# Optimization experiments

Hardware: AMD Instinct MI355X
Metric: run time of the kernel (lower is better)

The kernel has to match this reference:

```python
import jax, jax.numpy as jnp
import numpy as np

# Each of the 16 soft logic gates g(a,b) is affine in {1, a, b, a*b}.
# COEFF[g] = [k0, ka, kb, kab] so that gate_g = k0 + ka*a + kb*b + kab*a*b.
COEFF = np.array([
    [0,  0,  0,  0],   # 0: False
    [0,  0,  0,  1],   # 1: a AND b
    [0,  1,  0, -1],   # 2: a AND NOT b
    [0,  1,  0,  0],   # 3: a
    [0,  0,  1, -1],   # 4: NOT a AND b
    [0,  0,  1,  0],   # 5: b
    [0,  1,  1, -2],   # 6: XOR
    [0,  1,  1, -1],   # 7: OR
    [1, -1, -1,  1],   # 8: NOR
    [1, -1, -1,  2],   # 9: XNOR
    [1,  0, -1,  0],   # 10: NOT b
    [1,  0, -1,  1],   # 11: a OR NOT b
    [1, -1,  0,  0],   # 12: NOT a
    [1, -1,  0,  1],   # 13: NOT a OR b
    [1,  0,  0, -1],   # 14: NAND
    [1,  0,  0,  0],   # 15: True
], dtype=np.float32)

BATCH, IN_DIM, OUT_DIM, N_GATES = 2048, 16384, 16384, 16


def setup_inputs() -> dict:
    key = jax.random.key(0)
    k1, k2, k3, k4 = jax.random.split(key, 4)
    x = jax.random.uniform(k1, (BATCH, IN_DIM), dtype=jnp.float32)
    weights = jax.random.normal(k2, (OUT_DIM, N_GATES), dtype=jnp.float32)
    idx_a = jax.random.randint(k3, (OUT_DIM,), 0, IN_DIM, dtype=jnp.int64)
    idx_b = jax.random.randint(k4, (OUT_DIM,), 0, IN_DIM, dtype=jnp.int64)
    return {"x": x, "weights": weights, "idx_a": idx_a, "idx_b": idx_b}


def reference(x, weights, idx_a, idx_b):
    # Training-mode forward: softmax mixture over the 16 logic gates.
    nw = jax.nn.softmax(weights, axis=-1)            # [out, 16]
    W = nw @ jnp.asarray(COEFF, dtype=x.dtype)       # [out, 4] effective affine coeffs
    a = x[:, idx_a]                                  # [batch, out]
    b = x[:, idx_b]                                  # [batch, out]
    ab = a * b
    # r = sum_g nw[:,g] * gate_g(a,b) == W0 + Wa*a + Wb*b + Wab*ab
    return W[:, 0] + W[:, 1] * a + W[:, 2] * b + W[:, 3] * ab
```

## Files before the change

kernel.cpp:

```cpp
#include <hip/hip_runtime.h>

#define BATCH   2048
#define IN_DIM  16384
#define OUT_DIM 16384
#define NGATES  16

typedef float    f32x4 __attribute__((ext_vector_type(4)));
typedef _Float16 f16x4 __attribute__((ext_vector_type(4)));
typedef _Float16 f16x8 __attribute__((ext_vector_type(8)));

__constant__ float c_coeff[NGATES][4] = {
    {0, 0, 0, 0},  {0, 0, 0, 1},  {0, 1, 0, -1}, {0, 1, 0, 0},
    {0, 0, 1, -1}, {0, 0, 1, 0},  {0, 1, 1, -2}, {0, 1, 1, -1},
    {1, -1, -1, 1},{1, -1, -1, 2},{1, 0, -1, 0}, {1, 0, -1, 1},
    {1, -1, 0, 0}, {1, -1, 0, 1}, {1, 0, 0, -1}, {1, 0, 0, 0}
};

__global__ __launch_bounds__(256) void prep_kernel(
    const float* __restrict__ weights,
    const int*   __restrict__ idx_a,
    const int*   __restrict__ idx_b,
    f16x4*       __restrict__ Wh,
    unsigned*    __restrict__ Ipk)
{
    int j = blockIdx.x * blockDim.x + threadIdx.x;
    if (j >= OUT_DIM) return;

    const float4* wrow = reinterpret_cast<const float4*>(weights + (size_t)j * NGATES);
    float v[NGATES];
    float4 q0 = wrow[0], q1 = wrow[1], q2 = wrow[2], q3 = wrow[3];
    v[0]=q0.x; v[1]=q0.y; v[2]=q0.z; v[3]=q0.w;
    v[4]=q1.x; v[5]=q1.y; v[6]=q1.z; v[7]=q1.w;
    v[8]=q2.x; v[9]=q2.y; v[10]=q2.z; v[11]=q2.w;
    v[12]=q3.x; v[13]=q3.y; v[14]=q3.z; v[15]=q3.w;

    float m = v[0];
#pragma unroll
    for (int g = 1; g < NGATES; ++g) m = fmaxf(m, v[g]);
    float s = 0.f;
#pragma unroll
    for (int g = 0; g < NGATES; ++g) { v[g] = expf(v[g] - m); s += v[g]; }
    float inv = 1.0f / s;

    float c0 = 0.f, c1 = 0.f, c2 = 0.f, c3 = 0.f;
#pragma unroll
    for (int g = 0; g < NGATES; ++g) {
        c0 += v[g] * c_coeff[g][0];
        c1 += v[g] * c_coeff[g][1];
        c2 += v[g] * c_coeff[g][2];
        c3 += v[g] * c_coeff[g][3];
    }
    f16x4 h;
    h.x = (_Float16)(c0 * inv); h.y = (_Float16)(c1 * inv);
    h.z = (_Float16)(c2 * inv); h.w = (_Float16)(c3 * inv);
    Wh[j] = h;
    Ipk[j] = (unsigned)idx_a[j] | ((unsigned)idx_b[j] << 16);
}

__global__ __launch_bounds__(512, 8) void logic_row_kernel(
    const float* __restrict__ x,
    const f16x8* __restrict__ Wh8,
    const uint4* __restrict__ Ipk4,
    float*       __restrict__ out)
{
    __shared__ _Float16 rowh[IN_DIM];
    const int tid = threadIdx.x;
    const int i   = blockIdx.x;

    const f32x4* xr  = reinterpret_cast<const f32x4*>(x + (size_t)i * IN_DIM);
    f16x4*       rhw = reinterpret_cast<f16x4*>(rowh);
#pragma unroll
    for (int k = 0; k < IN_DIM / 4 / 512; ++k) {
        f32x4 v = xr[tid + k * 512];
        f16x4 h;
        h.x = (_Float16)v.x; h.y = (_Float16)v.y;
        h.z = (_Float16)v.z; h.w = (_Float16)v.w;
        rhw[tid + k * 512] = h;
    }

    uint4 qc = Ipk4[tid];
    f16x8 wa = Wh8[(size_t)tid * 2];
    f16x8 wb = Wh8[(size_t)tid * 2 + 1];

    __syncthreads();

    f32x4* o4 = reinterpret_cast<f32x4*>(out + (size_t)i * OUT_DIM);

    for (int k = 0; k < OUT_DIM / 4 / 512; ++k) {
        uint4 qn;  f16x8 wan, wbn;
        if (k + 1 < OUT_DIM / 4 / 512) {
            const int j4n = tid + (k + 1) * 512;
            qn  = Ipk4[j4n];
            wan = Wh8[(size_t)j4n * 2];
            wbn = Wh8[(size_t)j4n * 2 + 1];
        }

        float a0 = (float)rowh[qc.x & 0xFFFFu], b0 = (float)rowh[qc.x >> 16];
        float a1 = (float)rowh[qc.y & 0xFFFFu], b1 = (float)rowh[qc.y >> 16];
        float a2 = (float)rowh[qc.z & 0xFFFFu], b2 = (float)rowh[qc.z >> 16];
        float a3 = (float)rowh[qc.w & 0xFFFFu], b3 = (float)rowh[qc.w >> 16];

        f32x4 res;
        res.x = (float)wa[0] + (float)wa[1] * a0 + (float)wa[2] * b0 + (float)wa[3] * (a0 * b0);
        res.y = (float)wa[4] + (float)wa[5] * a1 + (float)wa[6] * b1 + (float)wa[7] * (a1 * b1);
        res.z = (float)wb[0] + (float)wb[1] * a2 + (float)wb[2] * b2 + (float)wb[3] * (a2 * b2);
        res.w = (float)wb[4] + (float)wb[5] * a3 + (float)wb[6] * b3 + (float)wb[7] * (a3 * b3);
        __builtin_nontemporal_store(res, &o4[tid + k * 512]);

        qc = qn; wa = wan; wb = wbn;
    }
}

extern "C" void kernel_launch(void* const* d_in, const int* in_sizes, int n_in,
                              void* d_out, int out_size, void* d_ws, size_t ws_size,
                              hipStream_t stream) {
    const float* x       = (const float*)d_in[0];
    const float* weights = (const float*)d_in[1];
    const int*   idx_a   = (const int*)d_in[2];
    const int*   idx_b   = (const int*)d_in[3];
    float* out = (float*)d_out;

    f16x4*    Wh  = (f16x4*)d_ws;
    unsigned* Ipk = (unsigned*)((char*)d_ws + (size_t)OUT_DIM * sizeof(f16x4));

    prep_kernel<<<(OUT_DIM + 255) / 256, 256, 0, stream>>>(weights, idx_a, idx_b, Wh, Ipk);
    logic_row_kernel<<<BATCH, 512, 0, stream>>>(x, (const f16x8*)Wh, (const uint4*)Ipk, out);
}
```

Before: 49.14 us.

## Process two rows per block, prefetching the next x row during compute

Each block now handles two batch rows. The second row of x is loaded into registers while the first row is being computed, and the converted fp16 row is reused from LDS. The grid shrinks to half as many blocks, and the compute loop is now fully unrolled. The aim is to hide the global load latency of the x row behind gather compute. In exchange, register pressure rises (8 f32x4 held across compute_row), which may cut occupancy under launch_bounds(512,8), and the kernel exposes less parallelism.

```diff
diff --git a/kernel.cpp b/kernel.cpp
--- a/kernel.cpp
+++ b/kernel.cpp
@@ -4,6 +4,8 @@
 #define IN_DIM  16384
 #define OUT_DIM 16384
 #define NGATES  16
+#define ROWS_PER_BLOCK 2
+#define NBLK (BATCH / ROWS_PER_BLOCK)
 
 typedef float    f32x4 __attribute__((ext_vector_type(4)));
 typedef _Float16 f16x4 __attribute__((ext_vector_type(4)));
@@ -57,35 +59,18 @@
     Ipk[j] = (unsigned)idx_a[j] | ((unsigned)idx_b[j] << 16);
 }
 
-__global__ __launch_bounds__(512, 8) void logic_row_kernel(
-    const float* __restrict__ x,
+__device__ __forceinline__ void compute_row(
+    const _Float16* __restrict__ rowh,
     const f16x8* __restrict__ Wh8,
     const uint4* __restrict__ Ipk4,
-    float*       __restrict__ out)
+    float* __restrict__ orow, int tid)
 {
-    __shared__ _Float16 rowh[IN_DIM];
-    const int tid = threadIdx.x;
-    const int i   = blockIdx.x;
-
-    const f32x4* xr  = reinterpret_cast<const f32x4*>(x + (size_t)i * IN_DIM);
-    f16x4*       rhw = reinterpret_cast<f16x4*>(rowh);
-#pragma unroll
-    for (int k = 0; k < IN_DIM / 4 / 512; ++k) {
-        f32x4 v = xr[tid + k * 512];
-        f16x4 h;
-        h.x = (_Float16)v.x; h.y = (_Float16)v.y;
-        h.z = (_Float16)v.z; h.w = (_Float16)v.w;
-        rhw[tid + k * 512] = h;
-    }
-
     uint4 qc = Ipk4[tid];
     f16x8 wa = Wh8[(size_t)tid * 2];
     f16x8 wb = Wh8[(size_t)tid * 2 + 1];
+    f32x4* o4 = reinterpret_cast<f32x4*>(orow);
 
-    __syncthreads();
-
-    f32x4* o4 = reinterpret_cast<f32x4*>(out + (size_t)i * OUT_DIM);
-
+#pragma unroll
     for (int k = 0; k < OUT_DIM / 4 / 512; ++k) {
         uint4 qn;  f16x8 wan, wbn;
         if (k + 1 < OUT_DIM / 4 / 512) {
@@ -111,6 +96,55 @@
     }
 }
 
+__global__ __launch_bounds__(512, 8) void logic_row_kernel(
+    const float* __restrict__ x,
+    const f16x8* __restrict__ Wh8,
+    const uint4* __restrict__ Ipk4,
+    float*       __restrict__ out)
+{
+    __shared__ _Float16 rowh[IN_DIM];
+    const int tid = threadIdx.x;
+    const int r0  = blockIdx.x * ROWS_PER_BLOCK;
+
+    f16x4* rhw = reinterpret_cast<f16x4*>(rowh);
+    f32x4  s[8];
+
+    {
+        const f32x4* xr = reinterpret_cast<const f32x4*>(x + (size_t)r0 * IN_DIM);
+#pragma unroll
+        for (int k = 0; k < 8; ++k) s[k] = xr[tid + k * 512];
+#pragma unroll
+        for (int k = 0; k < 8; ++k) {
+            f16x4 h;
+            h.x = (_Float16)s[k].x; h.y = (_Float16)s[k].y;
+            h.z = (_Float16)s[k].z; h.w = (_Float16)s[k].w;
+            rhw[tid + k * 512] = h;
+        }
+    }
+    __syncthreads();
+
+    {
+        const f32x4* xr = reinterpret_cast<const f32x4*>(x + (size_t)(r0 + 1) * IN_DIM);
+#pragma unroll
+        for (int k = 0; k < 8; ++k) s[k] = xr[tid + k * 512];
+    }
+
+    compute_row(rowh, Wh8, Ipk4, out + (size_t)r0 * OUT_DIM, tid);
+
+    __syncthreads();
+
+#pragma unroll
+    for (int k = 0; k < 8; ++k) {
+        f16x4 h;
+        h.x = (_Float16)s[k].x; h.y = (_Float16)s[k].y;
+        h.z = (_Float16)s[k].z; h.w = (_Float16)s[k].w;
+        rhw[tid + k * 512] = h;
+    }
+    __syncthreads();
+
+    compute_row(rowh, Wh8, Ipk4, out + (size_t)(r0 + 1) * OUT_DIM, tid);
+}
+
 extern "C" void kernel_launch(void* const* d_in, const int* in_sizes, int n_in,
                               void* d_out, int out_size, void* d_ws, size_t ws_size,
                               hipStream_t stream) {
@@ -124,5 +158,5 @@
     unsigned* Ipk = (unsigned*)((char*)d_ws + (size_t)OUT_DIM * sizeof(f16x4));
 
     prep_kernel<<<(OUT_DIM + 255) / 256, 256, 0, stream>>>(weights, idx_a, idx_b, Wh, Ipk);
-    logic_row_kernel<<<BATCH, 512, 0, stream>>>(x, (const f16x8*)Wh, (const uint4*)Ipk, out);
+    logic_row_kernel<<<NBLK, 512, 0, stream>>>(x, (const f16x8*)Wh, (const uint4*)Ipk, out);
 }
```

After: 56.74 us. +15.5%, slower.

## Double-buffer x rows in LDS with async global_load_lds across rows

Applied to the files above, without the earlier changes.

Each block now processes 8 batch rows with 1024 threads. It stages the next x row into a second LDS buffer using direct global-to-LDS loads while the current row is gathered and computed. Rows are kept in fp32 in LDS, which drops the fp16 conversion but doubles LDS use to 128KB per block, and the grid shrinks to 256 blocks. The per-block Wh/Ipk loads are amortised over rows, but occupancy and block count drop sharply. Barrier timing around the async loads could also be fragile.

```diff
diff --git a/kernel.cpp b/kernel.cpp
--- a/kernel.cpp
+++ b/kernel.cpp
@@ -4,6 +4,8 @@
 #define IN_DIM  16384
 #define OUT_DIM 16384
 #define NGATES  16
+#define ROWS_PER_BLOCK 8
+#define NBLK (BATCH / ROWS_PER_BLOCK)
 
 typedef float    f32x4 __attribute__((ext_vector_type(4)));
 typedef _Float16 f16x4 __attribute__((ext_vector_type(4)));
@@ -57,57 +59,77 @@
     Ipk[j] = (unsigned)idx_a[j] | ((unsigned)idx_b[j] << 16);
 }
 
-__global__ __launch_bounds__(512, 8) void logic_row_kernel(
-    const float* __restrict__ x,
+__device__ __forceinline__ void stage_row_async(const float* __restrict__ xrow,
+                                                float* lbuf, int tid)
+{
+#pragma unroll
+    for (int kk = 0; kk < 4; ++kk) {
+        __builtin_amdgcn_global_load_lds(
+            (const __attribute__((address_space(1))) void*)(xrow + tid * 4 + kk * 4096),
+            (__attribute__((address_space(3))) void*)(lbuf + tid * 4 + kk * 4096),
+            16, 0, 0);
+    }
+}
+
+__device__ __forceinline__ void compute_row(
+    const float* __restrict__ rowf,
     const f16x8* __restrict__ Wh8,
     const uint4* __restrict__ Ipk4,
-    float*       __restrict__ out)
+    float* __restrict__ orow, int tid)
 {
-    __shared__ _Float16 rowh[IN_DIM];
-    const int tid = threadIdx.x;
-    const int i   = blockIdx.x;
-
-    const f32x4* xr  = reinterpret_cast<const f32x4*>(x + (size_t)i * IN_DIM);
-    f16x4*       rhw = reinterpret_cast<f16x4*>(rowh);
-#pragma unroll
-    for (int k = 0; k < IN_DIM / 4 / 512; ++k) {
-        f32x4 v = xr[tid + k * 512];
-        f16x4 h;
-        h.x = (_Float16)v.x; h.y = (_Float16)v.y;
-        h.z = (_Float16)v.z; h.w = (_Float16)v.w;
-        rhw[tid + k * 512] = h;
-    }
-
     uint4 qc = Ipk4[tid];
     f16x8 wa = Wh8[(size_t)tid * 2];
     f16x8 wb = Wh8[(size_t)tid * 2 + 1];
+    f32x4* o4 = reinterpret_cast<f32x4*>(orow);
 
-    __syncthreads();
-
-    f32x4* o4 = reinterpret_cast<f32x4*>(out + (size_t)i * OUT_DIM);
-
-    for (int k = 0; k < OUT_DIM / 4 / 512; ++k) {
+#pragma unroll
+    for (int k = 0; k < OUT_DIM / 4 / 1024; ++k) {
         uint4 qn;  f16x8 wan, wbn;
-        if (k + 1 < OUT_DIM / 4 / 512) {
-            const int j4n = tid + (k + 1) * 512;
+        if (k + 1 < OUT_DIM / 4 / 1024) {
+            const int j4n = tid + (k + 1) * 1024;
             qn  = Ipk4[j4n];
             wan = Wh8[(size_t)j4n * 2];
             wbn = Wh8[(size_t)j4n * 2 + 1];
         }
 
-        float a0 = (float)rowh[qc.x & 0xFFFFu], b0 = (float)rowh[qc.x >> 16];
-        float a1 = (float)rowh[qc.y & 0xFFFFu], b1 = (float)rowh[qc.y >> 16];
-        float a2 = (float)rowh[qc.z & 0xFFFFu], b2 = (float)rowh[qc.z >> 16];
-        float a3 = (float)rowh[qc.w & 0xFFFFu], b3 = (float)rowh[qc.w >> 16];
+        float a0 = rowf[qc.x & 0xFFFFu], b0 = rowf[qc.x >> 16];
+        float a1 = rowf[qc.y & 0xFFFFu], b1 = rowf[qc.y >> 16];
+        float a2 = rowf[qc.z & 0xFFFFu], b2 = rowf[qc.z >> 16];
+        float a3 = rowf[qc.w & 0xFFFFu], b3 = rowf[qc.w >> 16];
 
         f32x4 res;
         res.x = (float)wa[0] + (float)wa[1] * a0 + (float)wa[2] * b0 + (float)wa[3] * (a0 * b0);
         res.y = (float)wa[4] + (float)wa[5] * a1 + (float)wa[6] * b1 + (float)wa[7] * (a1 * b1);
         res.z = (float)wb[0] + (float)wb[1] * a2 + (float)wb[2] * b2 + (float)wb[3] * (a2 * b2);
         res.w = (float)wb[4] + (float)wb[5] * a3 + (float)wb[6] * b3 + (float)wb[7] * (a3 * b3);
-        __builtin_nontemporal_store(res, &o4[tid + k * 512]);
+        __builtin_nontemporal_store(res, &o4[tid + k * 1024]);
 
         qc = qn; wa = wan; wb = wbn;
+    }
+}
+
+__global__ __launch_bounds__(1024, 2) void logic_row_kernel(
+    const float* __restrict__ x,
+    const f16x8* __restrict__ Wh8,
+    const uint4* __restrict__ Ipk4,
+    float*       __restrict__ out)
+{
+    __shared__ float buf[2][IN_DIM];
+    const int tid = threadIdx.x;
+    const int r0  = blockIdx.x * ROWS_PER_BLOCK;
+
+    stage_row_async(x + (size_t)r0 * IN_DIM, buf[0], tid);
+    asm volatile("s_waitcnt vmcnt(0)" ::: "memory");
+    __builtin_amdgcn_s_barrier();
+
+    for (int r = 0; r < ROWS_PER_BLOCK; ++r) {
+        if (r + 1 < ROWS_PER_BLOCK)
+            stage_row_async(x + (size_t)(r0 + r + 1) * IN_DIM, buf[(r + 1) & 1], tid);
+
+        compute_row(buf[r & 1], Wh8, Ipk4, out + (size_t)(r0 + r) * OUT_DIM, tid);
+
+        asm volatile("s_waitcnt vmcnt(0)" ::: "memory");
+        __builtin_amdgcn_s_barrier();
     }
 }
 
@@ -124,5 +146,5 @@
     unsigned* Ipk = (unsigned*)((char*)d_ws + (size_t)OUT_DIM * sizeof(f16x4));
 
     prep_kernel<<<(OUT_DIM + 255) / 256, 256, 0, stream>>>(weights, idx_a, idx_b, Wh, Ipk);
-    logic_row_kernel<<<BATCH, 512, 0, stream>>>(x, (const f16x8*)Wh, (const uint4*)Ipk, out);
+    logic_row_kernel<<<NBLK, 1024, 0, stream>>>(x, (const f16x8*)Wh, (const uint4*)Ipk, out);
 }
```

After: 78.72 us. 1.6x slower.

## Process four rows per block with double-buffered LDS row prefetch

Applied to the files above, without the earlier changes.

Each block now handles four batch rows instead of one and keeps two f16 row buffers in shared memory. While computing outputs for the current row, it loads the next x row from global memory, converts it, and stores it into the other buffer, so the global load overlaps with the gather work. This cuts the grid to a quarter of the blocks and doubles LDS per block, which lowers the occupancy hint to 4 blocks per CU. The trade is fewer resident waves and more register pressure in exchange for hiding the row-load latency.

```diff
diff --git a/kernel.cpp b/kernel.cpp
--- a/kernel.cpp
+++ b/kernel.cpp
@@ -4,6 +4,8 @@
 #define IN_DIM  16384
 #define OUT_DIM 16384
 #define NGATES  16
+#define ROWS_PER_BLOCK 4
+#define NBLK (BATCH / ROWS_PER_BLOCK)
 
 typedef float    f32x4 __attribute__((ext_vector_type(4)));
 typedef _Float16 f16x4 __attribute__((ext_vector_type(4)));
@@ -15,6 +17,13 @@
     {1, -1, -1, 1},{1, -1, -1, 2},{1, 0, -1, 0}, {1, 0, -1, 1},
     {1, -1, 0, 0}, {1, -1, 0, 1}, {1, 0, 0, -1}, {1, 0, 0, 0}
 };
+
+__device__ __forceinline__ f16x4 cvt_f16x4(f32x4 v) {
+    f16x4 h;
+    h.x = (_Float16)v.x; h.y = (_Float16)v.y;
+    h.z = (_Float16)v.z; h.w = (_Float16)v.w;
+    return h;
+}
 
 __global__ __launch_bounds__(256) void prep_kernel(
     const float* __restrict__ weights,
@@ -57,57 +66,71 @@
     Ipk[j] = (unsigned)idx_a[j] | ((unsigned)idx_b[j] << 16);
 }
 
-__global__ __launch_bounds__(512, 8) void logic_row_kernel(
+__global__ __launch_bounds__(512, 4) void logic_row_kernel(
     const float* __restrict__ x,
     const f16x8* __restrict__ Wh8,
     const uint4* __restrict__ Ipk4,
     float*       __restrict__ out)
 {
-    __shared__ _Float16 rowh[IN_DIM];
+    __shared__ _Float16 buf[2][IN_DIM];
     const int tid = threadIdx.x;
-    const int i   = blockIdx.x;
+    const int r0  = blockIdx.x * ROWS_PER_BLOCK;
 
-    const f32x4* xr  = reinterpret_cast<const f32x4*>(x + (size_t)i * IN_DIM);
-    f16x4*       rhw = reinterpret_cast<f16x4*>(rowh);
+    {
+        const f32x4* xr  = reinterpret_cast<const f32x4*>(x + (size_t)r0 * IN_DIM);
+        f16x4*       dst = reinterpret_cast<f16x4*>(buf[0]);
 #pragma unroll
-    for (int k = 0; k < IN_DIM / 4 / 512; ++k) {
-        f32x4 v = xr[tid + k * 512];
-        f16x4 h;
-        h.x = (_Float16)v.x; h.y = (_Float16)v.y;
-        h.z = (_Float16)v.z; h.w = (_Float16)v.w;
-        rhw[tid + k * 512] = h;
+        for (int k = 0; k < 8; ++k)
+            dst[tid + k * 512] = cvt_f16x4(xr[tid + k * 512]);
     }
-
-    uint4 qc = Ipk4[tid];
-    f16x8 wa = Wh8[(size_t)tid * 2];
-    f16x8 wb = Wh8[(size_t)tid * 2 + 1];
-
     __syncthreads();
 
-    f32x4* o4 = reinterpret_cast<f32x4*>(out + (size_t)i * OUT_DIM);
+    for (int r = 0; r < ROWS_PER_BLOCK; ++r) {
+        const _Float16* __restrict__ rowh = buf[r & 1];
+        f16x4* nb = reinterpret_cast<f16x4*>(buf[(r + 1) & 1]);
+        const bool more = (r + 1 < ROWS_PER_BLOCK);
+        const f32x4* xn = reinterpret_cast<const f32x4*>(
+            x + (size_t)(r0 + r + 1) * IN_DIM);
 
-    for (int k = 0; k < OUT_DIM / 4 / 512; ++k) {
-        uint4 qn;  f16x8 wan, wbn;
-        if (k + 1 < OUT_DIM / 4 / 512) {
-            const int j4n = tid + (k + 1) * 512;
-            qn  = Ipk4[j4n];
-            wan = Wh8[(size_t)j4n * 2];
-            wbn = Wh8[(size_t)j4n * 2 + 1];
+        uint4 qc = Ipk4[tid];
+        f16x8 wa = Wh8[(size_t)tid * 2];
+        f16x8 wb = Wh8[(size_t)tid * 2 + 1];
+        f32x4* o4 = reinterpret_cast<f32x4*>(out + (size_t)(r0 + r) * OUT_DIM);
+        f32x4 vprev;
+
+#pragma unroll
+        for (int k = 0; k < 8; ++k) {
+            f32x4 vcur;
+            if (more) vcur = xn[tid + k * 512];
+
+            uint4 qn;  f16x8 wan, wbn;
+            if (k + 1 < 8) {
+                const int j4n = tid + (k + 1) * 512;
+                qn  = Ipk4[j4n];
+                wan = Wh8[(size_t)j4n * 2];
+                wbn = Wh8[(size_t)j4n * 2 + 1];
+            }
+
+            float a0 = (float)rowh[qc.x & 0xFFFFu], b0 = (float)rowh[qc.x >> 16];
+            float a1 = (float)rowh[qc.y & 0xFFFFu], b1 = (float)rowh[qc.y >> 16];
+            float a2 = (float)rowh[qc.z & 0xFFFFu], b2 = (float)rowh[qc.z >> 16];
+            float a3 = (float)rowh[qc.w & 0xFFFFu], b3 = (float)rowh[qc.w >> 16];
+
+            f32x4 res;
+            res.x = (float)wa[0] + (float)wa[1] * a0 + (float)wa[2] * b0 + (float)wa[3] * (a0 * b0);
+            res.y = (float)wa[4] + (float)wa[5] * a1 + (float)wa[6] * b1 + (float)wa[7] * (a1 * b1);
+            res.z = (float)wb[0] + (float)wb[1] * a2 + (float)wb[2] * b2 + (float)wb[3] * (a2 * b2);
+            res.w = (float)wb[4] + (float)wb[5] * a3 + (float)wb[6] * b3 + (float)wb[7] * (a3 * b3);
+            __builtin_nontemporal_store(res, &o4[tid + k * 512]);
+
+            if (more && k > 0) nb[tid + (k - 1) * 512] = cvt_f16x4(vprev);
+            vprev = vcur;
+
+            qc = qn; wa = wan; wb = wbn;
         }
+        if (more) nb[tid + 7 * 512] = cvt_f16x4(vprev);
 
-        float a0 = (float)rowh[qc.x & 0xFFFFu], b0 = (float)rowh[qc.x >> 16];
-        float a1 = (float)rowh[qc.y & 0xFFFFu], b1 = (float)rowh[qc.y >> 16];
-        float a2 = (float)rowh[qc.z & 0xFFFFu], b2 = (float)rowh[qc.z >> 16];
-        float a3 = (float)rowh[qc.w & 0xFFFFu], b3 = (float)rowh[qc.w >> 16];
-
-        f32x4 res;
-        res.x = (float)wa[0] + (float)wa[1] * a0 + (float)wa[2] * b0 + (float)wa[3] * (a0 * b0);
-        res.y = (float)wa[4] + (float)wa[5] * a1 + (float)wa[6] * b1 + (float)wa[7] * (a1 * b1);
-        res.z = (float)wb[0] + (float)wb[1] * a2 + (float)wb[2] * b2 + (float)wb[3] * (a2 * b2);
-        res.w = (float)wb[4] + (float)wb[5] * a3 + (float)wb[6] * b3 + (float)wb[7] * (a3 * b3);
-        __builtin_nontemporal_store(res, &o4[tid + k * 512]);
-
-        qc = qn; wa = wan; wb = wbn;
+        __syncthreads();
     }
 }
 
@@ -124,5 +147,5 @@
     unsigned* Ipk = (unsigned*)((char*)d_ws + (size_t)OUT_DIM * sizeof(f16x4));
 
     prep_kernel<<<(OUT_DIM + 255) / 256, 256, 0, stream>>>(weights, idx_a, idx_b, Wh, Ipk);
-    logic_row_kernel<<<BATCH, 512, 0, stream>>>(x, (const f16x8*)Wh, (const uint4*)Ipk, out);
+    logic_row_kernel<<<NBLK, 512, 0, stream>>>(x, (const f16x8*)Wh, (const uint4*)Ipk, out);
 }
```

After: 51.32 us. 1.04x slower.
